# Optimization experiments

Measured on AMD Instinct MI355X. Metric: run time of the kernel, lower is better.

## Reference

```python
import jax, jax.numpy as jnp
import numpy as np

H = 512

def setup_inputs() -> dict:
    key = jax.random.key(0)
    ks = jax.random.split(key, 10)
    T, B, S = 64, 8, 512
    scale = 1.0 / np.sqrt(H)
    return {
        "attn_dec_state": jax.random.normal(ks[0], (T, B, H), jnp.float32),
        "attn_enc_state": jax.random.normal(ks[1], (S, B, H), jnp.float32),
        "attn_coverage": jax.random.uniform(ks[2], (B, S), jnp.float32),
        "Wq": jax.random.normal(ks[3], (H, H), jnp.float32) * scale,   # linear_query weight (in,out)
        "bq": jnp.zeros((H,), jnp.float32),
        "Wc": jax.random.normal(ks[4], (H, H), jnp.float32) * scale,   # linear_context weight
        "v": jax.random.normal(ks[5], (H,), jnp.float32) * scale,       # v projection H->1
        "Wo": jax.random.normal(ks[6], (2 * H, H), jnp.float32) * scale,  # linear_out weight
        "bo": jnp.zeros((H,), jnp.float32),
        "wcov": jax.random.normal(ks[7], (H,), jnp.float32) * scale,    # linear_cover weight 1->H
    }

def reference(attn_dec_state, attn_enc_state, attn_coverage, Wq, bq, Wc, v, Wo, bo, wcov):
    dec = jnp.transpose(attn_dec_state, (1, 0, 2))   # [B,T,H]
    enc = jnp.transpose(attn_enc_state, (1, 0, 2))   # [B,S,H]
    # coverage: linear_cover(1->H) applied to each scalar, added to enc, then tanh
    enc = jnp.tanh(enc + attn_coverage[:, :, None] * wcov)  # [B,S,H]
    # additive (Bahdanau) score with broadcast-tanh
    a1 = jnp.einsum('bth,hk->btk', dec, Wq) + bq             # [B,T,H]
    a2 = jnp.einsum('bsh,hk->bsk', enc, Wc)                  # [B,S,H]
    scores = jnp.einsum('btsh,h->bts', jnp.tanh(a1[:, :, None, :] + a2[:, None, :, :]), v)  # [B,T,S]
    align = jax.nn.softmax(scores, axis=-1)                  # [B,T,S]
    c = jnp.einsum('bts,bsh->bth', align, enc)               # [B,T,H]
    concat = jnp.concatenate([c, dec], axis=-1)              # [B,T,2H]
    attn_h = jnp.einsum('btd,dk->btk', concat, Wo) + bo      # [B,T,H]
    attn_h = jnp.transpose(attn_h, (1, 0, 2))                # [T,B,H]
    align_out = jnp.transpose(align, (1, 0, 2))              # [T,B,S]
    return attn_h, align_out
```

## Files before the change

### kernel.cpp

```cpp
#include <hip/hip_runtime.h>
#include <cstddef>

static constexpr int TT = 64;
static constexpr int BB = 8;
static constexpr int SS = 512;
static constexpr int HH = 512;

typedef __attribute__((ext_vector_type(8))) short bf16x8;
typedef __attribute__((ext_vector_type(4))) float f32x4;

__device__ __forceinline__ float fast_tanh(float x) {
  float e = __expf(2.0f * x);
  return 1.0f - 2.0f * __builtin_amdgcn_rcpf(e + 1.0f);
}
__device__ __forceinline__ unsigned short f2bf(float f) {
  unsigned u = __float_as_uint(f);
  return (unsigned short)((u + 0x7FFFu + ((u >> 16) & 1u)) >> 16);
}

__global__ __launch_bounds__(256)
void k_prep(const float* __restrict__ enc, const float* __restrict__ cov,
            const float* __restrict__ wcov, const float* __restrict__ dec,
            const float* __restrict__ Wq, const float* __restrict__ Wc,
            const float* __restrict__ Wo,
            unsigned short* __restrict__ encpb, unsigned short* __restrict__ concatb,
            unsigned short* __restrict__ WqT, unsigned short* __restrict__ WcT,
            unsigned short* __restrict__ WoT) {
  __shared__ float tile[32][33];
  const int blk = blockIdx.x, tid = threadIdx.x;

  if (blk < 8192) {
    const int idx = blk * 256 + tid;
    const int h = idx & 511;
    const int bs = idx >> 9;
    const int s = bs & 511, b = bs >> 9;
    const float x = enc[(size_t)(s * BB + b) * HH + h] + cov[bs] * wcov[h];
    encpb[idx] = f2bf(fast_tanh(x));
  } else if (blk < 8704) {
    const int m = blk - 8192, t = m & 63, b = m >> 6;
    const float2 dv = *(const float2*)(dec + (size_t)(t * BB + b) * HH + 2 * tid);
    ((unsigned*)concatb)[(size_t)m * 512 + 256 + tid] =
        (unsigned)f2bf(dv.x) | ((unsigned)f2bf(dv.y) << 16);
  } else {
    int l = blk - 8704;
    const float* W; unsigned short* WT; int KT;
    if (l < 256)      { W = Wq; WT = WqT; KT = 512; }
    else if (l < 512) { W = Wc; WT = WcT; KT = 512; l -= 256; }
    else              { W = Wo; WT = WoT; KT = 1024; l -= 512; }
    const int n0 = (l & 15) * 32, k0 = (l >> 4) * 32;
    const int r = tid >> 3, c4 = (tid & 7) * 4;
    const float4 w = *(const float4*)(W + (size_t)(k0 + r) * 512 + n0 + c4);
    tile[r][c4 + 0] = w.x; tile[r][c4 + 1] = w.y;
    tile[r][c4 + 2] = w.z; tile[r][c4 + 3] = w.w;
    __syncthreads();
    unsigned short* o = WT + (size_t)(n0 + r) * KT + k0 + c4;
#pragma unroll
    for (int i = 0; i < 4; ++i) o[i] = f2bf(tile[c4 + i][r]);
  }
}

template<int LDA, int LDB>
__device__ __forceinline__ void gemm_tile(const unsigned short* __restrict__ A,
                                          const unsigned short* __restrict__ BT,
                                          int m0, int n0, int kbeg, int kend,
                                          unsigned short (*As)[72],
                                          unsigned short (*Bs)[72],
                                          f32x4 acc[4]) {
  const int tid = threadIdx.x, w = tid >> 6, lane = tid & 63;
  const int lr = tid >> 2, lk = (tid & 3) * 16;
  const int fm = w * 16 + (lane & 15), fk = (lane >> 4) * 8;
  for (int k0 = kbeg; k0 < kend; k0 += 64) {
    const uint4* ga = (const uint4*)(A + (size_t)(m0 + lr) * LDA + k0 + lk);
    const uint4* gb = (const uint4*)(BT + (size_t)(n0 + lr) * LDB + k0 + lk);
    uint4 a0 = ga[0], a1 = ga[1], b0 = gb[0], b1 = gb[1];
    *(uint4*)&As[lr][lk] = a0;  *(uint4*)&As[lr][lk + 8] = a1;
    *(uint4*)&Bs[lr][lk] = b0;  *(uint4*)&Bs[lr][lk + 8] = b1;
    __syncthreads();
#pragma unroll
    for (int ks = 0; ks < 2; ++ks) {
      bf16x8 af = *(const bf16x8*)&As[fm][ks * 32 + fk];
#pragma unroll
      for (int j = 0; j < 4; ++j) {
        bf16x8 bf = *(const bf16x8*)&Bs[j * 16 + (lane & 15)][ks * 32 + fk];
        acc[j] = __builtin_amdgcn_mfma_f32_16x16x32_bf16(af, bf, acc[j], 0, 0, 0);
      }
    }
    __syncthreads();
  }
}

__global__ __launch_bounds__(256)
void k_gemm12(const unsigned short* __restrict__ concatb,
              const unsigned short* __restrict__ encpb,
              const unsigned short* __restrict__ WqT,
              const unsigned short* __restrict__ WcT,
              const unsigned short* __restrict__ WoT,
              const float* __restrict__ bq, const float* __restrict__ bo,
              float* __restrict__ Ea1, float* __restrict__ Ea2,
              float* __restrict__ attn_h) {
  __shared__ unsigned short As[64][72];
  __shared__ unsigned short Bs[64][72];
  const int g = blockIdx.x, tid = threadIdx.x;
  const int w = tid >> 6, lane = tid & 63;
  const int col = lane & 15, rq = lane >> 4;

  if (g < 64) {
    const int m0 = (g >> 3) * 64, n0 = (g & 7) * 64;
    f32x4 acc[4] = {};
    gemm_tile<1024, 512>(concatb + 512, WqT, m0, n0, 0, 512, As, Bs, acc);
#pragma unroll
    for (int j = 0; j < 4; ++j) {
      const int n = n0 + j * 16 + col;
      const float bv = bq[n];
#pragma unroll
      for (int r = 0; r < 4; ++r) {
        const int m = m0 + w * 16 + rq * 4 + r;
        float val = fminf(fmaxf(acc[j][r] + bv, -30.0f), 30.0f);
        Ea1[(size_t)m * 512 + n] = __expf(2.0f * val);
      }
    }
  } else if (g < 576) {
    const int u = g - 64;
    const int m0 = (u >> 3) * 64, n0 = (u & 7) * 64;
    f32x4 acc[4] = {};
    gemm_tile<512, 512>(encpb, WcT, m0, n0, 0, 512, As, Bs, acc);
#pragma unroll
    for (int j = 0; j < 4; ++j) {
      const int n = n0 + j * 16 + col;
#pragma unroll
      for (int r = 0; r < 4; ++r) {
        const int m = m0 + w * 16 + rq * 4 + r;
        float val = fminf(fmaxf(acc[j][r], -30.0f), 30.0f);
        Ea2[(size_t)m * 512 + n] = __expf(2.0f * val);
      }
    }
  } else {
    const int u = g - 576;
    const int m0 = (u >> 3) * 64, n0 = (u & 7) * 64;
    f32x4 acc[4] = {};
    gemm_tile<1024, 1024>(concatb, WoT, m0, n0, 512, 1024, As, Bs, acc);
#pragma unroll
    for (int j = 0; j < 4; ++j) {
      const int n = n0 + j * 16 + col;
      const float bv = bo[n];
#pragma unroll
      for (int r = 0; r < 4; ++r) {
        const int m = m0 + w * 16 + rq * 4 + r;
        const int bi = m >> 6, t = m & 63;
        attn_h[(size_t)(t * BB + bi) * 512 + n] = acc[j][r] + bv;
      }
    }
  }
}

__global__ __launch_bounds__(512)
void k_attn(const float* __restrict__ Ea1, const float* __restrict__ Ea2,
            const float* __restrict__ v, const unsigned short* __restrict__ encpb,
            float* __restrict__ align_out, unsigned short* __restrict__ concatb) {
  __shared__ __align__(16) char smem[12352];
  float (*sc)[512]   = (float(*)[512])smem;
  float (*ea1s)[512] = (float(*)[512])(smem + 4096);
  float* v2s         = (float*)(smem + 8192);
  float2* part       = (float2*)(smem + 4096);
  float (*red)[8]    = (float(*)[8])(smem + 12288);

  const int g = blockIdx.x, tid = threadIdx.x;
  const int b = g & 7, t0 = (g >> 3) * 2;
  const int wv = tid >> 6, lane = tid & 63;
  const int hq = lane & 3, sl = lane >> 2;

  ea1s[0][tid] = Ea1[(size_t)(b * TT + t0) * HH + tid];
  ea1s[1][tid] = Ea1[(size_t)(b * TT + t0 + 1) * HH + tid];
  v2s[tid] = 2.0f * v[tid];
  __syncthreads();

#define TERM(E1, E2, VV, A) A = fmaf(VV, __builtin_amdgcn_rcpf(fmaf(E1, E2, 1.0f)), A)
  for (int p = 0; p < 2; ++p) {
    const int s0 = p * 256 + wv * 32 + sl;
    const float* e2p0 = Ea2 + (size_t)(b * SS + s0) * HH;
    const float* e2p1 = e2p0 + (size_t)16 * HH;
    float acc[2][2] = {};
#pragma unroll 4
    for (int it = 0; it < 32; ++it) {
      const int h = it * 16 + hq * 4;
      const float4 e20 = *(const float4*)(e2p0 + h);
      const float4 e21 = *(const float4*)(e2p1 + h);
      const float4 vvv = *(const float4*)&v2s[h];
      float4 e1r[2];
      e1r[0] = *(const float4*)&ea1s[0][h];
      e1r[1] = *(const float4*)&ea1s[1][h];
#pragma unroll
      for (int i = 0; i < 2; ++i) {
        TERM(e1r[i].x, e20.x, vvv.x, acc[i][0]);
        TERM(e1r[i].y, e20.y, vvv.y, acc[i][0]);
        TERM(e1r[i].z, e20.z, vvv.z, acc[i][0]);
        TERM(e1r[i].w, e20.w, vvv.w, acc[i][0]);
        TERM(e1r[i].x, e21.x, vvv.x, acc[i][1]);
        TERM(e1r[i].y, e21.y, vvv.y, acc[i][1]);
        TERM(e1r[i].z, e21.z, vvv.z, acc[i][1]);
        TERM(e1r[i].w, e21.w, vvv.w, acc[i][1]);
      }
    }
#pragma unroll
    for (int i = 0; i < 2; ++i)
#pragma unroll
      for (int j = 0; j < 2; ++j) {
        acc[i][j] += __shfl_xor(acc[i][j], 1);
        acc[i][j] += __shfl_xor(acc[i][j], 2);
      }
    if (hq == 0) {
      sc[0][s0] = -acc[0][0]; sc[0][s0 + 16] = -acc[0][1];
      sc[1][s0] = -acc[1][0]; sc[1][s0 + 16] = -acc[1][1];
    }
  }
#undef TERM
  __syncthreads();

  const float x0 = sc[0][tid], x1 = sc[1][tid];
  float m0 = x0, m1 = x1;
#pragma unroll
  for (int off = 32; off; off >>= 1) {
    m0 = fmaxf(m0, __shfl_xor(m0, off));
    m1 = fmaxf(m1, __shfl_xor(m1, off));
  }
  if (lane == 0) { red[0][wv] = m0; red[1][wv] = m1; }
  __syncthreads();
  m0 = red[0][0]; m1 = red[1][0];
#pragma unroll
  for (int w2 = 1; w2 < 8; ++w2) { m0 = fmaxf(m0, red[0][w2]); m1 = fmaxf(m1, red[1][w2]); }
  __syncthreads();
  const float e0 = __expf(x0 - m0), e1 = __expf(x1 - m1);
  float s0v = e0, s1v = e1;
#pragma unroll
  for (int off = 32; off; off >>= 1) {
    s0v += __shfl_xor(s0v, off);
    s1v += __shfl_xor(s1v, off);
  }
  if (lane == 0) { red[0][wv] = s0v; red[1][wv] = s1v; }
  __syncthreads();
  float sum0 = 0.f, sum1 = 0.f;
#pragma unroll
  for (int w2 = 0; w2 < 8; ++w2) { sum0 += red[0][w2]; sum1 += red[1][w2]; }
  const float a0 = e0 * __builtin_amdgcn_rcpf(sum0);
  const float a1 = e1 * __builtin_amdgcn_rcpf(sum1);

  align_out[(size_t)(t0 + 0) * BB * SS + b * SS + tid] = a0;
  align_out[(size_t)(t0 + 1) * BB * SS + b * SS + tid] = a1;
  sc[0][tid] = a0;
  sc[1][tid] = a1;
  __syncthreads();

  {
    const int sh = tid >> 8, hp = tid & 255;
    const unsigned* ep = (const unsigned*)encpb + (size_t)b * SS * 256;
    float c00 = 0.f, c01 = 0.f, c10 = 0.f, c11 = 0.f;
#pragma unroll 8
    for (int s2 = sh * 256; s2 < sh * 256 + 256; ++s2) {
      const unsigned u = ep[s2 * 256 + hp];
      const float elo = __uint_as_float(u << 16);
      const float ehi = __uint_as_float(u & 0xffff0000u);
      const float av0 = sc[0][s2], av1 = sc[1][s2];
      c00 = fmaf(av0, elo, c00); c01 = fmaf(av0, ehi, c01);
      c10 = fmaf(av1, elo, c10); c11 = fmaf(av1, ehi, c11);
    }
    part[(0 * 2 + sh) * 256 + hp] = make_float2(c00, c01);
    part[(1 * 2 + sh) * 256 + hp] = make_float2(c10, c11);
  }
  __syncthreads();
  {
    const int t = tid >> 8, hp = tid & 255;
    const float2 pa = part[(t * 2 + 0) * 256 + hp];
    const float2 pb = part[(t * 2 + 1) * 256 + hp];
    const float clo = pa.x + pb.x, chi = pa.y + pb.y;
    ((unsigned*)concatb)[(size_t)(b * TT + t0 + t) * 512 + hp] =
        (unsigned)f2bf(clo) | ((unsigned)f2bf(chi) << 16);
  }
}

__global__ __launch_bounds__(256)
void k_out(const unsigned short* __restrict__ A,
           const unsigned short* __restrict__ BT,
           float* __restrict__ C) {
  __shared__ unsigned short As[64][72];
  __shared__ unsigned short Bs[64][72];
  const int tid = threadIdx.x;
  const int w = tid >> 6, lane = tid & 63;
  const int tau = blockIdx.x >> 2, kc = blockIdx.x & 3;
  const int n0 = (tau & 7) * 64, m0 = (tau >> 3) * 64;

  f32x4 acc[4] = {};
  gemm_tile<1024, 1024>(A, BT, m0, n0, kc * 128, kc * 128 + 128, As, Bs, acc);

  const int col = lane & 15, rq = lane >> 4;
#pragma unroll
  for (int j = 0; j < 4; ++j) {
    const int n = n0 + j * 16 + col;
#pragma unroll
    for (int r = 0; r < 4; ++r) {
      const int m = m0 + w * 16 + rq * 4 + r;
      const int bi = m >> 6, t = m & 63;
      unsafeAtomicAdd(&C[(size_t)(t * BB + bi) * 512 + n], acc[j][r]);
    }
  }
}

extern "C" void kernel_launch(void* const* d_in, const int* in_sizes, int n_in,
                              void* d_out, int out_size, void* d_ws, size_t ws_size,
                              hipStream_t stream) {
  const float* dec  = (const float*)d_in[0];
  const float* enc  = (const float*)d_in[1];
  const float* cov  = (const float*)d_in[2];
  const float* Wq   = (const float*)d_in[3];
  const float* bq   = (const float*)d_in[4];
  const float* Wc   = (const float*)d_in[5];
  const float* v    = (const float*)d_in[6];
  const float* Wo   = (const float*)d_in[7];
  const float* bo   = (const float*)d_in[8];
  const float* wcov = (const float*)d_in[9];

  float* out = (float*)d_out;
  float* attn_h    = out;
  float* align_out = out + (size_t)TT * BB * HH;

  char* w = (char*)d_ws;
  const size_t MB = 1024 * 1024;
  unsigned short* encpb   = (unsigned short*)(w);
  unsigned short* WqT     = (unsigned short*)(w + 4 * MB);
  unsigned short* WcT     = (unsigned short*)(w + 4 * MB + 512 * 1024);
  unsigned short* WoT     = (unsigned short*)(w + 5 * MB);
  unsigned short* concatb = (unsigned short*)(w + 6 * MB);
  float*          Ea1     = (float*)(w + 7 * MB);
  float*          Ea2     = (float*)(w + 8 * MB);

  k_prep<<<9728, 256, 0, stream>>>(enc, cov, wcov, dec, Wq, Wc, Wo,
                                   encpb, concatb, WqT, WcT, WoT);
  k_gemm12<<<640, 256, 0, stream>>>(concatb, encpb, WqT, WcT, WoT, bq, bo,
                                    Ea1, Ea2, attn_h);
  k_attn<<<256, 512, 0, stream>>>(Ea1, Ea2, v, encpb, align_out, concatb);
  k_out<<<256, 256, 0, stream>>>(concatb, WoT, attn_h);
}
```

Baseline: 132.9 us.

## Vectorize prep, pair reciprocals in score loop, double attention block size

The prep kernel now converts four elements per thread with float4 loads and ushort4 stores, cutting its block count. The score loop merges two reciprocal terms into one using a common denominator, v1/x1 + v2/x2 = (v1*x2 + v2*x1)/(x1*x2), which halves the rcp instructions. The clamp is tightened to ±10.5 so the product of the two denominators cannot overflow. The attention kernel runs 1024 threads per block, with each thread handling one score pass instead of two, and the context reduction is split four ways. This trades transcendental throughput for a few extra multiplies and some precision risk.

```diff
diff --git a/kernel.cpp b/kernel.cpp
--- a/kernel.cpp
+++ b/kernel.cpp
@@ -29,20 +29,28 @@
   __shared__ float tile[32][33];
   const int blk = blockIdx.x, tid = threadIdx.x;
 
-  if (blk < 8192) {
-    const int idx = blk * 256 + tid;
-    const int h = idx & 511;
-    const int bs = idx >> 9;
+  if (blk < 2048) {
+    const int r = tid >> 7, c = (tid & 127) * 4;
+    const int bs = blk * 2 + r;
     const int s = bs & 511, b = bs >> 9;
-    const float x = enc[(size_t)(s * BB + b) * HH + h] + cov[bs] * wcov[h];
-    encpb[idx] = f2bf(fast_tanh(x));
-  } else if (blk < 8704) {
-    const int m = blk - 8192, t = m & 63, b = m >> 6;
-    const float2 dv = *(const float2*)(dec + (size_t)(t * BB + b) * HH + 2 * tid);
-    ((unsigned*)concatb)[(size_t)m * 512 + 256 + tid] =
-        (unsigned)f2bf(dv.x) | ((unsigned)f2bf(dv.y) << 16);
+    const float4 ev = *(const float4*)(enc + (size_t)(s * BB + b) * HH + c);
+    const float cv = cov[bs];
+    const float4 wv = *(const float4*)(wcov + c);
+    ushort4 o;
+    o.x = f2bf(fast_tanh(ev.x + cv * wv.x));
+    o.y = f2bf(fast_tanh(ev.y + cv * wv.y));
+    o.z = f2bf(fast_tanh(ev.z + cv * wv.z));
+    o.w = f2bf(fast_tanh(ev.w + cv * wv.w));
+    *(ushort4*)(encpb + (size_t)bs * HH + c) = o;
+  } else if (blk < 2304) {
+    const int r = tid >> 7, c = (tid & 127) * 4;
+    const int m = (blk - 2048) * 2 + r, t = m & 63, b = m >> 6;
+    const float4 dv = *(const float4*)(dec + (size_t)(t * BB + b) * HH + c);
+    ushort4 o;
+    o.x = f2bf(dv.x); o.y = f2bf(dv.y); o.z = f2bf(dv.z); o.w = f2bf(dv.w);
+    *(ushort4*)(concatb + (size_t)m * 1024 + 512 + c) = o;
   } else {
-    int l = blk - 8704;
+    int l = blk - 2304;
     const float* W; unsigned short* WT; int KT;
     if (l < 256)      { W = Wq; WT = WqT; KT = 512; }
     else if (l < 512) { W = Wc; WT = WcT; KT = 512; l -= 256; }
@@ -115,7 +123,7 @@
 #pragma unroll
       for (int r = 0; r < 4; ++r) {
         const int m = m0 + w * 16 + rq * 4 + r;
-        float val = fminf(fmaxf(acc[j][r] + bv, -30.0f), 30.0f);
+        float val = fminf(fmaxf(acc[j][r] + bv, -10.5f), 10.5f);
         Ea1[(size_t)m * 512 + n] = __expf(2.0f * val);
       }
     }
@@ -130,7 +138,7 @@
 #pragma unroll
       for (int r = 0; r < 4; ++r) {
         const int m = m0 + w * 16 + rq * 4 + r;
-        float val = fminf(fmaxf(acc[j][r], -30.0f), 30.0f);
+        float val = fminf(fmaxf(acc[j][r], -10.5f), 10.5f);
         Ea2[(size_t)m * 512 + n] = __expf(2.0f * val);
       }
     }
@@ -153,33 +161,42 @@
   }
 }
 
-__global__ __launch_bounds__(512)
+__global__ __launch_bounds__(1024)
 void k_attn(const float* __restrict__ Ea1, const float* __restrict__ Ea2,
             const float* __restrict__ v, const unsigned short* __restrict__ encpb,
             float* __restrict__ align_out, unsigned short* __restrict__ concatb) {
-  __shared__ __align__(16) char smem[12352];
+  __shared__ __align__(16) char smem[20544];
   float (*sc)[512]   = (float(*)[512])smem;
   float (*ea1s)[512] = (float(*)[512])(smem + 4096);
-  float* v2s         = (float*)(smem + 8192);
+  float* v2s         = (float*)(smem + 12288);
   float2* part       = (float2*)(smem + 4096);
-  float (*red)[8]    = (float(*)[8])(smem + 12288);
+  float (*red)[8]    = (float(*)[8])(smem + 20480);
 
   const int g = blockIdx.x, tid = threadIdx.x;
   const int b = g & 7, t0 = (g >> 3) * 2;
   const int wv = tid >> 6, lane = tid & 63;
   const int hq = lane & 3, sl = lane >> 2;
 
-  ea1s[0][tid] = Ea1[(size_t)(b * TT + t0) * HH + tid];
-  ea1s[1][tid] = Ea1[(size_t)(b * TT + t0 + 1) * HH + tid];
-  v2s[tid] = 2.0f * v[tid];
-  __syncthreads();
-
-#define TERM(E1, E2, VV, A) A = fmaf(VV, __builtin_amdgcn_rcpf(fmaf(E1, E2, 1.0f)), A)
-  for (int p = 0; p < 2; ++p) {
-    const int s0 = p * 256 + wv * 32 + sl;
+  if (tid < 512) {
+    ea1s[0][tid] = Ea1[(size_t)(b * TT + t0) * HH + tid];
+    ea1s[1][tid] = Ea1[(size_t)(b * TT + t0 + 1) * HH + tid];
+  } else {
+    v2s[tid - 512] = 2.0f * v[tid - 512];
+  }
+  __syncthreads();
+
+  const int s0 = wv * 32 + sl;
+  {
     const float* e2p0 = Ea2 + (size_t)(b * SS + s0) * HH;
     const float* e2p1 = e2p0 + (size_t)16 * HH;
     float acc[2][2] = {};
+#define PAIR(E1a, E2a, Va, E1b, E2b, Vb, A)                                  \
+    {                                                                        \
+      const float x1 = fmaf(E1a, E2a, 1.0f), x2 = fmaf(E1b, E2b, 1.0f);      \
+      const float rr = __builtin_amdgcn_rcpf(x1 * x2);                       \
+      const float nn = fmaf(Va, x2, Vb * x1);                                \
+      A = fmaf(nn, rr, A);                                                   \
+    }
 #pragma unroll 4
     for (int it = 0; it < 32; ++it) {
       const int h = it * 16 + hq * 4;
@@ -191,16 +208,13 @@
       e1r[1] = *(const float4*)&ea1s[1][h];
 #pragma unroll
       for (int i = 0; i < 2; ++i) {
-        TERM(e1r[i].x, e20.x, vvv.x, acc[i][0]);
-        TERM(e1r[i].y, e20.y, vvv.y, acc[i][0]);
-        TERM(e1r[i].z, e20.z, vvv.z, acc[i][0]);
-        TERM(e1r[i].w, e20.w, vvv.w, acc[i][0]);
-        TERM(e1r[i].x, e21.x, vvv.x, acc[i][1]);
-        TERM(e1r[i].y, e21.y, vvv.y, acc[i][1]);
-        TERM(e1r[i].z, e21.z, vvv.z, acc[i][1]);
-        TERM(e1r[i].w, e21.w, vvv.w, acc[i][1]);
-      }
-    }
+        PAIR(e1r[i].x, e20.x, vvv.x, e1r[i].y, e20.y, vvv.y, acc[i][0]);
+        PAIR(e1r[i].z, e20.z, vvv.z, e1r[i].w, e20.w, vvv.w, acc[i][0]);
+        PAIR(e1r[i].x, e21.x, vvv.x, e1r[i].y, e21.y, vvv.y, acc[i][1]);
+        PAIR(e1r[i].z, e21.z, vvv.z, e1r[i].w, e21.w, vvv.w, acc[i][1]);
+      }
+    }
+#undef PAIR
 #pragma unroll
     for (int i = 0; i < 2; ++i)
 #pragma unroll
@@ -213,49 +227,58 @@
       sc[1][s0] = -acc[1][0]; sc[1][s0 + 16] = -acc[1][1];
     }
   }
-#undef TERM
-  __syncthreads();
-
-  const float x0 = sc[0][tid], x1 = sc[1][tid];
-  float m0 = x0, m1 = x1;
-#pragma unroll
-  for (int off = 32; off; off >>= 1) {
-    m0 = fmaxf(m0, __shfl_xor(m0, off));
-    m1 = fmaxf(m1, __shfl_xor(m1, off));
-  }
-  if (lane == 0) { red[0][wv] = m0; red[1][wv] = m1; }
-  __syncthreads();
-  m0 = red[0][0]; m1 = red[1][0];
-#pragma unroll
-  for (int w2 = 1; w2 < 8; ++w2) { m0 = fmaxf(m0, red[0][w2]); m1 = fmaxf(m1, red[1][w2]); }
-  __syncthreads();
-  const float e0 = __expf(x0 - m0), e1 = __expf(x1 - m1);
-  float s0v = e0, s1v = e1;
-#pragma unroll
-  for (int off = 32; off; off >>= 1) {
-    s0v += __shfl_xor(s0v, off);
-    s1v += __shfl_xor(s1v, off);
-  }
-  if (lane == 0) { red[0][wv] = s0v; red[1][wv] = s1v; }
-  __syncthreads();
-  float sum0 = 0.f, sum1 = 0.f;
-#pragma unroll
-  for (int w2 = 0; w2 < 8; ++w2) { sum0 += red[0][w2]; sum1 += red[1][w2]; }
-  const float a0 = e0 * __builtin_amdgcn_rcpf(sum0);
-  const float a1 = e1 * __builtin_amdgcn_rcpf(sum1);
-
-  align_out[(size_t)(t0 + 0) * BB * SS + b * SS + tid] = a0;
-  align_out[(size_t)(t0 + 1) * BB * SS + b * SS + tid] = a1;
-  sc[0][tid] = a0;
-  sc[1][tid] = a1;
-  __syncthreads();
-
+  __syncthreads();
+
+  float x0 = 0.f, x1 = 0.f, e0 = 0.f, e1 = 0.f;
+  if (tid < 512) {
+    x0 = sc[0][tid]; x1 = sc[1][tid];
+    float m0 = x0, m1 = x1;
+#pragma unroll
+    for (int off = 32; off; off >>= 1) {
+      m0 = fmaxf(m0, __shfl_xor(m0, off));
+      m1 = fmaxf(m1, __shfl_xor(m1, off));
+    }
+    if (lane == 0) { red[0][wv] = m0; red[1][wv] = m1; }
+  }
+  __syncthreads();
   {
-    const int sh = tid >> 8, hp = tid & 255;
+    float m0 = red[0][0], m1 = red[1][0];
+#pragma unroll
+    for (int w2 = 1; w2 < 8; ++w2) { m0 = fmaxf(m0, red[0][w2]); m1 = fmaxf(m1, red[1][w2]); }
+    __syncthreads();
+    if (tid < 512) {
+      e0 = __expf(x0 - m0); e1 = __expf(x1 - m1);
+      float s0v = e0, s1v = e1;
+#pragma unroll
+      for (int off = 32; off; off >>= 1) {
+        s0v += __shfl_xor(s0v, off);
+        s1v += __shfl_xor(s1v, off);
+      }
+      if (lane == 0) { red[0][wv] = s0v; red[1][wv] = s1v; }
+    }
+  }
+  __syncthreads();
+  {
+    float sum0 = 0.f, sum1 = 0.f;
+#pragma unroll
+    for (int w2 = 0; w2 < 8; ++w2) { sum0 += red[0][w2]; sum1 += red[1][w2]; }
+    if (tid < 512) {
+      const float a0 = e0 * __builtin_amdgcn_rcpf(sum0);
+      const float a1 = e1 * __builtin_amdgcn_rcpf(sum1);
+      align_out[(size_t)(t0 + 0) * BB * SS + b * SS + tid] = a0;
+      align_out[(size_t)(t0 + 1) * BB * SS + b * SS + tid] = a1;
+      sc[0][tid] = a0;
+      sc[1][tid] = a1;
+    }
+  }
+  __syncthreads();
+
+  {
+    const int q = tid >> 8, hp = tid & 255;
     const unsigned* ep = (const unsigned*)encpb + (size_t)b * SS * 256;
     float c00 = 0.f, c01 = 0.f, c10 = 0.f, c11 = 0.f;
 #pragma unroll 8
-    for (int s2 = sh * 256; s2 < sh * 256 + 256; ++s2) {
+    for (int s2 = q * 128; s2 < q * 128 + 128; ++s2) {
       const unsigned u = ep[s2 * 256 + hp];
       const float elo = __uint_as_float(u << 16);
       const float ehi = __uint_as_float(u & 0xffff0000u);
@@ -263,15 +286,18 @@
       c00 = fmaf(av0, elo, c00); c01 = fmaf(av0, ehi, c01);
       c10 = fmaf(av1, elo, c10); c11 = fmaf(av1, ehi, c11);
     }
-    part[(0 * 2 + sh) * 256 + hp] = make_float2(c00, c01);
-    part[(1 * 2 + sh) * 256 + hp] = make_float2(c10, c11);
-  }
-  __syncthreads();
-  {
+    part[(0 * 4 + q) * 256 + hp] = make_float2(c00, c01);
+    part[(1 * 4 + q) * 256 + hp] = make_float2(c10, c11);
+  }
+  __syncthreads();
+  if (tid < 512) {
     const int t = tid >> 8, hp = tid & 255;
-    const float2 pa = part[(t * 2 + 0) * 256 + hp];
-    const float2 pb = part[(t * 2 + 1) * 256 + hp];
-    const float clo = pa.x + pb.x, chi = pa.y + pb.y;
+    float clo = 0.f, chi = 0.f;
+#pragma unroll
+    for (int q = 0; q < 4; ++q) {
+      const float2 p = part[(t * 4 + q) * 256 + hp];
+      clo += p.x; chi += p.y;
+    }
     ((unsigned*)concatb)[(size_t)(b * TT + t0 + t) * 512 + hp] =
         (unsigned)f2bf(clo) | ((unsigned)f2bf(chi) << 16);
   }
@@ -332,10 +358,10 @@
   float*          Ea1     = (float*)(w + 7 * MB);
   float*          Ea2     = (float*)(w + 8 * MB);
 
-  k_prep<<<9728, 256, 0, stream>>>(enc, cov, wcov, dec, Wq, Wc, Wo,
+  k_prep<<<3328, 256, 0, stream>>>(enc, cov, wcov, dec, Wq, Wc, Wo,
                                    encpb, concatb, WqT, WcT, WoT);
   k_gemm12<<<640, 256, 0, stream>>>(concatb, encpb, WqT, WcT, WoT, bq, bo,
                                     Ea1, Ea2, attn_h);
-  k_attn<<<256, 512, 0, stream>>>(Ea1, Ea2, v, encpb, align_out, concatb);
+  k_attn<<<256, 1024, 0, stream>>>(Ea1, Ea2, v, encpb, align_out, concatb);
   k_out<<<256, 256, 0, stream>>>(concatb, WoT, attn_h);
 }
```

Result: faster. 126.2 us (-5.0%).
